# Kernel optimization log

Hardware: AMD Instinct MI355X
Metric: run time of the kernel (lower is better)

Reference implementation:

```python
import jax, jax.numpy as jnp
import numpy as np
import math

B, L, D = 2, 2048, 768
H, DK = 8, 64
DV = D // H  # 96
N_POS = 32
DFF = 2 * D
EPS = 1e-5


def setup_inputs() -> dict:
    key = jax.random.key(0)
    ks = jax.random.split(key, 12)
    s = 0.02
    return {
        "x": jax.random.normal(ks[0], (B, L, D), jnp.float32),
        "norm1_w": jnp.ones((D,), jnp.float32),
        "norm2_w": jnp.ones((D,), jnp.float32),
        "wq": jax.random.normal(ks[1], (D, H * DK), jnp.float32) * s,
        "wk": jax.random.normal(ks[2], (D, H * DK), jnp.float32) * s,
        "wv": jax.random.normal(ks[3], (D, H * DV), jnp.float32) * s,
        "wo": jax.random.normal(ks[4], (H * DV, D), jnp.float32) * s,
        "bo": jnp.zeros((D,), jnp.float32),
        "u_param": jax.random.normal(ks[5], (H, DK), jnp.float32) * s,
        "v_param": jax.random.normal(ks[6], (H, DK), jnp.float32) * s,
        "w_pos": jax.random.normal(ks[7], (H, DK, N_POS), jnp.float32) * s,
        "w1": jax.random.normal(ks[8], (D, DFF), jnp.float32) * s,
        "b1": jnp.zeros((DFF,), jnp.float32),
        "w2": jax.random.normal(ks[9], (DFF, D), jnp.float32) * s,
        "b2": jnp.zeros((D,), jnp.float32),
    }


def _rel_basis(l: int, n: int) -> jnp.ndarray:
    # Enformer-style central-mask relative position basis: [l, l, n]
    pos = jnp.arange(l)
    distance = pos[None, :] - pos[:, None]  # [l, l]
    pow_rate = jnp.exp(jnp.log(jnp.float32((l + 1) / 2.0)) / (n // 2))
    center_widths = pow_rate ** jnp.arange(1, n // 2 + 1, dtype=jnp.float32)
    d = distance[:, :, None].astype(jnp.float32)
    unsigned = (jnp.abs(d) <= center_widths).astype(jnp.float32)
    signed = jnp.sign(d) * unsigned
    return jnp.concatenate([unsigned, signed], axis=-1)  # [l, l, n]


def _rmsnorm(x, w):
    norm = jnp.mean(x * x, axis=-1, keepdims=True)
    return x * jax.lax.rsqrt(norm + EPS) * w


def reference(x, norm1_w, norm2_w, wq, wk, wv, wo, bo,
              u_param, v_param, w_pos, w1, b1, w2, b2):
    b, l, _ = x.shape
    skip = x
    h1 = _rmsnorm(x, norm1_w)

    q = (h1 @ wq).reshape(b, l, H, DK)
    k = (h1 @ wk).reshape(b, l, H, DK)
    v = (h1 @ wv).reshape(b, l, H, DV)

    basis = _rel_basis(l, N_POS)  # [l, l, n]
    scale = 1.0 / math.sqrt(DK)

    # qr_term: contract q with w_pos first, then with basis (avoids [h,l,l,d] r)
    qw = jnp.einsum('bihd,hdn->bihn', q, w_pos)          # [b,l,h,n]
    qr = jnp.einsum('bihn,ijn->bhij', qw, basis)          # [b,h,l,l]
    uk = jnp.einsum('hd,bjhd->bhj', u_param, k)[:, :, None, :]  # [b,h,1,l]
    vw = jnp.einsum('hd,hdn->hn', v_param, w_pos)         # [h,n]
    vr = jnp.einsum('hn,ijn->hij', vw, basis)[None]       # [1,h,l,l]

    bias = (qr + uk + vr) * scale
    scores = jnp.einsum('bihd,bjhd->bhij', q, k) * scale + bias
    attn = jax.nn.softmax(scores, axis=-1)
    out = jnp.einsum('bhij,bjhd->bihd', attn, v)          # [b,l,h,dv]

    out = out.reshape(b, l, H * DV) @ wo + bo
    x = out + skip

    skip = x
    h2 = _rmsnorm(x, norm2_w)
    h2 = jax.nn.gelu(h2 @ w1 + b1, approximate=False) @ w2 + b2
    return h2 + skip
```

## Files before the change

kernel.cpp:

```cpp
#include <hip/hip_runtime.h>

#define B_ 2
#define L_ 2048
#define D_ 768
#define H_ 8
#define DK_ 64
#define DV_ 96
#define NPOS_ 32

typedef __attribute__((ext_vector_type(8))) __bf16 bf16x8;
typedef __attribute__((ext_vector_type(4))) __bf16 bf16x4;
typedef __attribute__((ext_vector_type(4))) float f32x4;

static __device__ __forceinline__ float bs2f(short s) {
    return (float)__builtin_bit_cast(__bf16, s);
}
static __device__ __forceinline__ short f2bs(float f) {
    return __builtin_bit_cast(short, (__bf16)f);
}

__global__ __launch_bounds__(256) void prep_kernel(
    const float* __restrict__ wq, const float* __restrict__ wk,
    const float* __restrict__ wv, const float* __restrict__ wo,
    const float* __restrict__ w1, const float* __restrict__ w2,
    const float* __restrict__ vparam, const float* __restrict__ uparam,
    const float* __restrict__ wpos,
    short* __restrict__ wqkvT, short* __restrict__ woT,
    short* __restrict__ w1T, short* __restrict__ w2T,
    unsigned char* __restrict__ sidx, float* __restrict__ VU, float* __restrict__ VS,
    const float* __restrict__ x, const float* __restrict__ n1w, short* __restrict__ h1)
{
    __shared__ short T[64][66];
    __shared__ float vw[H_ * NPOS_];
    __shared__ float uw[H_ * NPOS_];
    __shared__ float red[4];
    int blk = blockIdx.x, tid = threadIdx.x;
    if (blk < 1056) {
        const float* W; short* Wt; int K, N, bx, by;
        if (blk < 96)       { W = wq; Wt = wqkvT;              K = 768;  N = 512;  int b = blk;       bx = b % 8;  by = b / 8; }
        else if (blk < 192) { W = wk; Wt = wqkvT + 512 * 768;  K = 768;  N = 512;  int b = blk - 96;  bx = b % 8;  by = b / 8; }
        else if (blk < 336) { W = wv; Wt = wqkvT + 1024 * 768; K = 768;  N = 768;  int b = blk - 192; bx = b % 12; by = b / 12; }
        else if (blk < 480) { W = wo; Wt = woT;                K = 768;  N = 768;  int b = blk - 336; bx = b % 12; by = b / 12; }
        else if (blk < 768) { W = w1; Wt = w1T;                K = 768;  N = 1536; int b = blk - 480; bx = b % 24; by = b / 24; }
        else                { W = w2; Wt = w2T;                K = 1536; N = 768;  int b = blk - 768; bx = b % 12; by = b / 12; }
        int n0 = bx << 6, k0 = by << 6;
        for (int idx = tid; idx < 4096; idx += 256) {
            int r = idx >> 6, c = idx & 63;
            T[c][r] = f2bs(W[(size_t)(k0 + r) * N + n0 + c]);
        }
        __syncthreads();
        for (int idx = tid; idx < 4096; idx += 256) {
            int r = idx >> 6, c = idx & 63;
            Wt[(size_t)(n0 + r) * K + k0 + c] = T[r][c];
        }
    } else if (blk == 1056) {
        float pr = expf(logf((L_ + 1) / 2.0f) / (NPOS_ / 2));
        for (int idx = tid; idx < 4095; idx += 256) {
            int d = idx - 2047;
            int ad = d < 0 ? -d : d;
            int c = 0;
            for (int m = 1; m <= NPOS_ / 2; ++m) {
                float cw = powf(pr, (float)m);
                if (cw < (float)ad) c++;
            }
            sidx[idx] = (unsigned char)(d > 0 ? c : (d < 0 ? 17 + c : 34));
        }
        {
            int h = tid >> 5, n = tid & 31;
            float av = 0.f, au = 0.f;
            for (int d = 0; d < DK_; ++d) {
                float wp = wpos[(h * DK_ + d) * NPOS_ + n];
                av += vparam[h * DK_ + d] * wp;
                au += uparam[h * DK_ + d] * wp;
            }
            vw[tid] = av;
            uw[tid] = au;
        }
        __syncthreads();
        if (tid < H_ * 17) {
            int h = tid / 17, m = tid % 17;
            float su = 0.f, ss = 0.f;
            for (int t2 = m; t2 < 16; ++t2) {
                su += vw[h * NPOS_ + t2] - uw[h * NPOS_ + t2];
                ss += vw[h * NPOS_ + 16 + t2] - uw[h * NPOS_ + 16 + t2];
            }
            VU[h * 17 + m] = su * 0.125f;
            VS[h * 17 + m] = ss * 0.125f;
        }
    } else {
        int row = blk - 1057;
        const float* xr = x + (size_t)row * D_;
        float ss = 0.f;
        for (int c = tid; c < D_; c += 256) { float f = xr[c]; ss += f * f; }
        for (int msk = 1; msk < 64; msk <<= 1) ss += __shfl_xor(ss, msk);
        if ((tid & 63) == 0) red[tid >> 6] = ss;
        __syncthreads();
        float tot = red[0] + red[1] + red[2] + red[3];
        float sc = rsqrtf(tot * (1.f / D_) + 1e-5f);
        for (int c = tid; c < D_; c += 256)
            h1[(size_t)row * D_ + c] = f2bs(xr[c] * sc * n1w[c]);
    }
}

__global__ __launch_bounds__(256) void rmsnorm_kernel(
    const float* __restrict__ x, const float* __restrict__ wgt, short* __restrict__ out)
{
    int row = blockIdx.x, tid = threadIdx.x;
    __shared__ float red[4];
    const float* xr = x + (size_t)row * D_;
    float ss = 0.f;
    for (int c = tid; c < D_; c += 256) { float f = xr[c]; ss += f * f; }
    for (int msk = 1; msk < 64; msk <<= 1) ss += __shfl_xor(ss, msk);
    if ((tid & 63) == 0) red[tid >> 6] = ss;
    __syncthreads();
    float tot = red[0] + red[1] + red[2] + red[3];
    float sc = rsqrtf(tot * (1.f / D_) + 1e-5f);
    for (int c = tid; c < D_; c += 256)
        out[(size_t)row * D_ + c] = f2bs(xr[c] * sc * wgt[c]);
}

__global__ __launch_bounds__(256) void gemm64(
    const short* __restrict__ A, const short* __restrict__ Bt,
    const float* __restrict__ bias, const float* __restrict__ resid,
    void* __restrict__ outp,
    int M, int N, int K, int act, int out_f32)
{
    __shared__ __align__(16) short Al[64 * 136];
    __shared__ __align__(16) short Bl[64 * 136];
    int tid = threadIdx.x;
    int w = tid >> 6, lane = tid & 63, quad = lane >> 4, t = lane & 15;
    int m0b = blockIdx.y << 6, n0b = blockIdx.x << 6;
    int wr = (w >> 1) << 5, wc = (w & 1) << 5;
    int rA = tid >> 4, c8 = (tid & 15) << 3;
    f32x4 acc[2][2] = {};
    bf16x8 pA[4], pB[4];
#pragma unroll
    for (int it = 0; it < 4; ++it) {
        pA[it] = *(const bf16x8*)&A[(size_t)(m0b + rA + (it << 4)) * K + c8];
        pB[it] = *(const bf16x8*)&Bt[(size_t)(n0b + rA + (it << 4)) * K + c8];
    }
    for (int kb = 0; kb < K; kb += 128) {
        __syncthreads();
#pragma unroll
        for (int it = 0; it < 4; ++it) {
            *(bf16x8*)&Al[(rA + (it << 4)) * 136 + c8] = pA[it];
            *(bf16x8*)&Bl[(rA + (it << 4)) * 136 + c8] = pB[it];
        }
        if (kb + 128 < K) {
#pragma unroll
            for (int it = 0; it < 4; ++it) {
                pA[it] = *(const bf16x8*)&A[(size_t)(m0b + rA + (it << 4)) * K + kb + 128 + c8];
                pB[it] = *(const bf16x8*)&Bt[(size_t)(n0b + rA + (it << 4)) * K + kb + 128 + c8];
            }
        }
        __syncthreads();
#pragma unroll
        for (int ks = 0; ks < 4; ++ks) {
            bf16x8 af0 = *(bf16x8*)&Al[(wr + t) * 136 + (ks << 5) + (quad << 3)];
            bf16x8 af1 = *(bf16x8*)&Al[(wr + 16 + t) * 136 + (ks << 5) + (quad << 3)];
            bf16x8 bf0 = *(bf16x8*)&Bl[(wc + t) * 136 + (ks << 5) + (quad << 3)];
            bf16x8 bf1 = *(bf16x8*)&Bl[(wc + 16 + t) * 136 + (ks << 5) + (quad << 3)];
            acc[0][0] = __builtin_amdgcn_mfma_f32_16x16x32_bf16(af0, bf0, acc[0][0], 0, 0, 0);
            acc[0][1] = __builtin_amdgcn_mfma_f32_16x16x32_bf16(af0, bf1, acc[0][1], 0, 0, 0);
            acc[1][0] = __builtin_amdgcn_mfma_f32_16x16x32_bf16(af1, bf0, acc[1][0], 0, 0, 0);
            acc[1][1] = __builtin_amdgcn_mfma_f32_16x16x32_bf16(af1, bf1, acc[1][1], 0, 0, 0);
        }
    }
#pragma unroll
    for (int ms = 0; ms < 2; ++ms)
#pragma unroll
        for (int ns = 0; ns < 2; ++ns)
#pragma unroll
            for (int r = 0; r < 4; ++r) {
                int row = m0b + wr + (ms << 4) + (quad << 2) + r;
                int col = n0b + wc + (ns << 4) + t;
                float v2 = acc[ms][ns][r];
                if (bias) v2 += bias[col];
                if (act == 1) v2 = 0.5f * v2 * (1.f + erff(v2 * 0.70710678118654752f));
                if (resid) v2 += resid[(size_t)row * N + col];
                if (out_f32) ((float*)outp)[(size_t)row * N + col] = v2;
                else ((short*)outp)[(size_t)row * N + col] = f2bs(v2);
            }
}

__global__ __launch_bounds__(256) void gemm128(
    const short* __restrict__ A, const short* __restrict__ Bt,
    const float* __restrict__ bias, const float* __restrict__ uadd,
    void* __restrict__ outp, int M, int N, int K, int act)
{
    __shared__ __align__(16) short Al[128 * 72];
    __shared__ __align__(16) short Bl[128 * 72];
    int tid = threadIdx.x;
    int w = tid >> 6, lane = tid & 63, quad = lane >> 4, t = lane & 15;
    int m0b = blockIdx.y << 7, n0b = blockIdx.x << 7;
    int wm = (w >> 1) << 6, wn = (w & 1) << 6;
    int r0 = tid >> 3, c8 = (tid & 7) << 3;
    f32x4 acc[4][4] = {};
    bf16x8 pA[4], pB[4];
#pragma unroll
    for (int it = 0; it < 4; ++it) {
        pA[it] = *(const bf16x8*)&A[(size_t)(m0b + r0 + (it << 5)) * K + c8];
        pB[it] = *(const bf16x8*)&Bt[(size_t)(n0b + r0 + (it << 5)) * K + c8];
    }
    for (int kb = 0; kb < K; kb += 64) {
        __syncthreads();
#pragma unroll
        for (int it = 0; it < 4; ++it) {
            *(bf16x8*)&Al[(r0 + (it << 5)) * 72 + c8] = pA[it];
            *(bf16x8*)&Bl[(r0 + (it << 5)) * 72 + c8] = pB[it];
        }
        if (kb + 64 < K) {
#pragma unroll
            for (int it = 0; it < 4; ++it) {
                pA[it] = *(const bf16x8*)&A[(size_t)(m0b + r0 + (it << 5)) * K + kb + 64 + c8];
                pB[it] = *(const bf16x8*)&Bt[(size_t)(n0b + r0 + (it << 5)) * K + kb + 64 + c8];
            }
        }
        __syncthreads();
#pragma unroll
        for (int ks = 0; ks < 2; ++ks) {
            bf16x8 af[4], bf[4];
#pragma unroll
            for (int ms = 0; ms < 4; ++ms)
                af[ms] = *(bf16x8*)&Al[(wm + ms * 16 + t) * 72 + (ks << 5) + (quad << 3)];
#pragma unroll
            for (int ns = 0; ns < 4; ++ns)
                bf[ns] = *(bf16x8*)&Bl[(wn + ns * 16 + t) * 72 + (ks << 5) + (quad << 3)];
#pragma unroll
            for (int ms = 0; ms < 4; ++ms)
#pragma unroll
                for (int ns = 0; ns < 4; ++ns)
                    acc[ms][ns] = __builtin_amdgcn_mfma_f32_16x16x32_bf16(af[ms], bf[ns], acc[ms][ns], 0, 0, 0);
        }
    }
#pragma unroll
    for (int ms = 0; ms < 4; ++ms)
#pragma unroll
        for (int ns = 0; ns < 4; ++ns)
#pragma unroll
            for (int r = 0; r < 4; ++r) {
                int row = m0b + wm + ms * 16 + (quad << 2) + r;
                int col = n0b + wn + ns * 16 + t;
                float v2 = acc[ms][ns][r];
                if (uadd && col < 512) v2 = 0.125f * (v2 + uadd[col]);
                if (bias) v2 += bias[col];
                if (act == 1) v2 = 0.5f * v2 * (1.f + erff(v2 * 0.70710678118654752f));
                ((short*)outp)[(size_t)row * N + col] = f2bs(v2);
            }
}

__global__ __launch_bounds__(256) void qv_kernel(
    const short* __restrict__ qkv, const float* __restrict__ wpos,
    const float* __restrict__ VU, const float* __restrict__ VS,
    float* __restrict__ Tg, short* __restrict__ vT)
{
    __shared__ __align__(16) char arena[69696];
    int blk = blockIdx.x, tid = threadIdx.x;
    if (blk < 256) {
        float* wl   = (float*)arena;
        float* qrow = (float*)(arena + 65536);
        float* qw   = (float*)(arena + 67584);
        float* sU   = (float*)(arena + 68608);
        float* sS   = (float*)(arena + 69152);
        for (int idx = tid; idx < 4096; idx += 256)
            ((float4*)wl)[idx] = ((const float4*)wpos)[idx];
        int r0 = blk << 4;
        int h = tid >> 5, n = tid & 31;
        for (int rr = 0; rr < 16; ++rr) {
            int row = r0 + rr;
            __syncthreads();
            const short* base = qkv + (size_t)row * 1792;
            qrow[tid]       = bs2f(base[tid]);
            qrow[tid + 256] = bs2f(base[tid + 256]);
            __syncthreads();
            float acc = 0.f;
            for (int d = 0; d < DK_; ++d)
                acc += qrow[h * DK_ + d] * wl[(h * DK_ + d) * 32 + n];
            qw[tid] = acc;
            __syncthreads();
            if (tid < 136) {
                int hh = tid / 17, m = tid % 17;
                float su = 0.f, ss = 0.f;
                for (int t2 = m; t2 < 16; ++t2) { su += qw[hh * NPOS_ + t2]; ss += qw[hh * NPOS_ + 16 + t2]; }
                sU[tid] = su + VU[tid];
                sS[tid] = ss + VS[tid];
            }
            __syncthreads();
            if (tid < 280) {
                int h2 = tid / 35, s = tid % 35;
                int m = s < 17 ? s : (s < 34 ? s - 17 : 0);
                float su = sU[h2 * 17 + m], ss = sS[h2 * 17 + m];
                Tg[(size_t)row * 280 + tid] = s < 17 ? su + ss : (s < 34 ? su - ss : su);
            }
        }
    } else {
        short* T = (short*)arena;
        int vb = blk - 256;
        int bh = vb >> 4, b = bh >> 3, h = bh & 7;
        int j0 = (vb & 15) << 7;
#pragma unroll
        for (int it = 0; it < 6; ++it) {
            int idx = tid + (it << 8);
            int row = idx / 12, c8 = (idx % 12) << 3;
            *(bf16x8*)&T[row * 104 + c8] =
                *(const bf16x8*)&qkv[(size_t)(b * L_ + j0 + row) * 1792 + 1024 + h * DV_ + c8];
        }
        __syncthreads();
#pragma unroll
        for (int it = 0; it < 6; ++it) {
            int idx = tid + (it << 8);
            int sub = idx / 768;
            int rem = idx - sub * 768;
            int f = rem >> 6, l = rem & 63;
            int dv = f >> 1, ks = f & 1;
            int q = l >> 4, t = l & 15;
            bf16x8 o;
#pragma unroll
            for (int e = 0; e < 8; ++e) {
                int jl = ((e & 3) << 4) + (ks << 3) + (q << 1) + (e >> 2);
                o[e] = __builtin_bit_cast(__bf16, T[(sub * 64 + jl) * 104 + dv * 16 + t]);
            }
            int jt = ((vb & 15) << 1) + sub;
            *(bf16x8*)&vT[((((size_t)bh * 32 + jt) * 12 + f) * 64 + l) * 8] = o;
        }
    }
}

__global__ __launch_bounds__(512, 4) void flash_kernel(
    const short* __restrict__ qkv, const short* __restrict__ vT,
    const float* __restrict__ Tg, const unsigned char* __restrict__ sidx_g,
    short* __restrict__ ao)
{
    __shared__ __align__(16) char arena[50176];
    int tid = threadIdx.x;
    int w = tid >> 6, lane = tid & 63, quad = lane >> 4, t = lane & 15;
    int g = w >> 2, wg = w & 3, tg = tid & 255;
    short* Kl = (short*)(arena + g * 18432);
    short* Pl = (short*)(arena + g * 18432 + 9216);
    float* Tt = (float*)(arena + 36864);
    unsigned char* sidxl = (unsigned char*)(arena + 46080);
    int bh = blockIdx.y, b = bh >> 3, h = bh & 7;
    int i0 = blockIdx.x << 6;

    for (int idx = tid; idx < 64 * 35; idx += 512) {
        int il = idx / 35, s = idx % 35;
        Tt[il * 36 + s] = Tg[(size_t)(b * L_ + i0 + il) * 280 + h * 35 + s];
    }
    for (int idx = tid; idx < 4095; idx += 512) sidxl[idx] = sidx_g[idx];

    int iq = i0 + wg * 16 + t;
    const short* qbase = qkv + (size_t)(b * L_ + iq) * 1792 + h * DK_;
    bf16x8 qf0 = *(const bf16x8*)(qbase + (quad << 3));
    bf16x8 qf1 = *(const bf16x8*)(qbase + 32 + (quad << 3));

    f32x4 O[6] = {};
    float lsum[4] = {0.f, 0.f, 0.f, 0.f};

    int kr = tg >> 3, kc = (tg & 7) << 3;
    bf16x8 kpre[2];
    {
        int j0 = g << 6;
        const short* kb0 = &qkv[(size_t)(b * L_ + j0 + kr) * 1792 + 512 + h * DK_ + kc];
        kpre[0] = *(const bf16x8*)kb0;
        kpre[1] = *(const bf16x8*)(kb0 + (size_t)32 * 1792);
    }
    const short* vfb = vT + (size_t)bh * 32 * 12 * 512 + lane * 8;

    for (int tix = 0; tix < 16; ++tix) {
        int j0 = ((tix << 1) + g) << 6;
        int jt = j0 >> 6;
        __syncthreads();
        *(bf16x8*)&Kl[kr * 72 + kc] = kpre[0];
        *(bf16x8*)&Kl[(kr + 32) * 72 + kc] = kpre[1];
        bf16x8 vfrag[12];
#pragma unroll
        for (int f = 0; f < 12; ++f)
            vfrag[f] = *(const bf16x8*)(vfb + ((size_t)jt * 12 + f) * 512);
        {
            int jn = (tix < 15) ? ((((tix + 1) << 1) + g) << 6) : (g << 6);
            const short* kb0 = &qkv[(size_t)(b * L_ + jn + kr) * 1792 + 512 + h * DK_ + kc];
            kpre[0] = *(const bf16x8*)kb0;
            kpre[1] = *(const bf16x8*)(kb0 + (size_t)32 * 1792);
        }
        __syncthreads();

        f32x4 S[4];
        __builtin_amdgcn_s_setprio(1);
#pragma unroll
        for (int ct = 0; ct < 4; ++ct) {
            bf16x8 b0 = *(bf16x8*)&Kl[(ct * 16 + t) * 72 + (quad << 3)];
            bf16x8 b1 = *(bf16x8*)&Kl[(ct * 16 + t) * 72 + 32 + (quad << 3)];
            f32x4 z = {};
            z = __builtin_amdgcn_mfma_f32_16x16x32_bf16(qf0, b0, z, 0, 0, 0);
            S[ct] = __builtin_amdgcn_mfma_f32_16x16x32_bf16(qf1, b1, z, 0, 0, 0);
        }
        __builtin_amdgcn_s_setprio(0);
#pragma unroll
        for (int r = 0; r < 4; ++r) {
            int il = wg * 16 + (quad << 2) + r;
            int i = i0 + il;
            const float* Trow = &Tt[il * 36];
            bf16x4 pv;
#pragma unroll
            for (int ct = 0; ct < 4; ++ct) {
                int j = j0 + ct * 16 + t;
                int s = sidxl[j - i + 2047];
                float p = __expf(S[ct][r] + Trow[s]);
                __bf16 pb = (__bf16)p;
                pv[ct] = pb;
                lsum[r] += (float)pb;
            }
            *(bf16x4*)&Pl[il * 72 + t * 4] = pv;
        }
        __builtin_amdgcn_s_setprio(1);
#pragma unroll
        for (int ks = 0; ks < 2; ++ks) {
            bf16x8 pa = *(bf16x8*)&Pl[(wg * 16 + t) * 72 + (ks << 5) + (quad << 3)];
#pragma unroll
            for (int dv = 0; dv < 6; ++dv)
                O[dv] = __builtin_amdgcn_mfma_f32_16x16x32_bf16(pa, vfrag[dv * 2 + ks], O[dv], 0, 0, 0);
        }
        __builtin_amdgcn_s_setprio(0);
    }

    __syncthreads();
    float* F = (float*)arena;
    int l2 = (wg << 6) + lane;
    if (g == 1) {
#pragma unroll
        for (int dv = 0; dv < 6; ++dv)
#pragma unroll
            for (int r = 0; r < 4; ++r)
                F[((dv << 2) + r) * 256 + l2] = O[dv][r];
#pragma unroll
        for (int r = 0; r < 4; ++r) F[(24 + r) * 256 + l2] = lsum[r];
    }
    __syncthreads();
    if (g == 0) {
#pragma unroll
        for (int r = 0; r < 4; ++r) {
            float lr = lsum[r] + F[(24 + r) * 256 + l2];
            lr += __shfl_xor(lr, 1);
            lr += __shfl_xor(lr, 2);
            lr += __shfl_xor(lr, 4);
            lr += __shfl_xor(lr, 8);
            float inv = 1.f / lr;
            int i = i0 + wg * 16 + (quad << 2) + r;
            size_t base = (size_t)(b * L_ + i) * D_ + h * DV_;
#pragma unroll
            for (int dv = 0; dv < 6; ++dv)
                ao[base + dv * 16 + t] = f2bs((O[dv][r] + F[((dv << 2) + r) * 256 + l2]) * inv);
        }
    }
}

extern "C" void kernel_launch(void* const* d_in, const int* in_sizes, int n_in,
                              void* d_out, int out_size, void* d_ws, size_t ws_size,
                              hipStream_t stream)
{
    const float* x    = (const float*)d_in[0];
    const float* n1w  = (const float*)d_in[1];
    const float* n2w  = (const float*)d_in[2];
    const float* wq   = (const float*)d_in[3];
    const float* wk   = (const float*)d_in[4];
    const float* wv   = (const float*)d_in[5];
    const float* wo   = (const float*)d_in[6];
    const float* bo   = (const float*)d_in[7];
    const float* up   = (const float*)d_in[8];
    const float* vp   = (const float*)d_in[9];
    const float* wpos = (const float*)d_in[10];
    const float* w1   = (const float*)d_in[11];
    const float* b1   = (const float*)d_in[12];
    const float* w2   = (const float*)d_in[13];
    const float* b2   = (const float*)d_in[14];

    char* ws = (char*)d_ws;
    short* h1   = (short*)(ws + 0);
    short* qkv  = (short*)(ws + 6291456);
    float* Tg   = (float*)(ws + 20971520);
    float* VUg  = (float*)(ws + 25559040);
    float* VSg  = (float*)(ws + 25560064);
    unsigned char* sidx = (unsigned char*)(ws + 25561088);
    short* ao   = (short*)(ws + 25569280);
    float* x2   = (float*)(ws + 31860736);
    short* vT   = (short*)(ws + 31860736);
    short* wqkvT= (short*)(ws + 44443648);
    short* woT  = (short*)(ws + 47196160);
    short* w1T  = (short*)(ws + 48375808);
    short* w2T  = (short*)(ws + 50735104);
    short* f1   = (short*)(ws + 0);
    short* h2n  = (short*)(ws + 14680064);

    prep_kernel<<<5153, 256, 0, stream>>>(wq, wk, wv, wo, w1, w2, vp, up, wpos,
                                          wqkvT, woT, w1T, w2T, sidx, VUg, VSg,
                                          x, n1w, h1);
    gemm128<<<dim3(14, 32), 256, 0, stream>>>(h1, wqkvT, nullptr, up, qkv, 4096, 1792, 768, 0);
    qv_kernel<<<512, 256, 0, stream>>>(qkv, wpos, VUg, VSg, Tg, vT);
    flash_kernel<<<dim3(32, 16), 512, 0, stream>>>(qkv, vT, Tg, sidx, ao);
    gemm64<<<dim3(12, 64), 256, 0, stream>>>(ao, woT, bo, x, x2, 4096, 768, 768, 0, 1);
    rmsnorm_kernel<<<4096, 256, 0, stream>>>(x2, n2w, h2n);
    gemm128<<<dim3(12, 32), 256, 0, stream>>>(h2n, w1T, b1, nullptr, f1, 4096, 1536, 768, 1);
    gemm64<<<dim3(12, 64), 256, 0, stream>>>(f1, w2T, b2, x2, d_out, 4096, 768, 1536, 0, 1);
}
```

Baseline: 309.1 us.

## Pre-swizzle K into MFMA fragment layout and drop LDS staging in flash kernel

Adds a K-transpose pass to qv_kernel that writes K in MFMA B-fragment order, so flash_kernel loads K fragments straight from global memory instead of staging them through LDS. This removes the per-tile __syncthreads and LDS writes for K. The flash kernel also shrinks to 256 threads with 32 query rows per block and a swizzled 1D grid that interleaves heads. The costs are an extra global write/read pass for K, more redundant global K loads across blocks, and twice as many blocks.

```diff
diff --git a/kernel.cpp b/kernel.cpp
--- a/kernel.cpp
+++ b/kernel.cpp
@@ -252,7 +252,7 @@
 __global__ __launch_bounds__(256) void qv_kernel(
     const short* __restrict__ qkv, const float* __restrict__ wpos,
     const float* __restrict__ VU, const float* __restrict__ VS,
-    float* __restrict__ Tg, short* __restrict__ vT)
+    float* __restrict__ Tg, short* __restrict__ vT, short* __restrict__ kT)
 {
     __shared__ __align__(16) char arena[69696];
     int blk = blockIdx.x, tid = threadIdx.x;
@@ -293,7 +293,7 @@
                 Tg[(size_t)row * 280 + tid] = s < 17 ? su + ss : (s < 34 ? su - ss : su);
             }
         }
-    } else {
+    } else if (blk < 512) {
         short* T = (short*)arena;
         int vb = blk - 256;
         int bh = vb >> 4, b = bh >> 3, h = bh & 7;
@@ -323,83 +323,101 @@
             int jt = ((vb & 15) << 1) + sub;
             *(bf16x8*)&vT[((((size_t)bh * 32 + jt) * 12 + f) * 64 + l) * 8] = o;
         }
-    }
-}
-
-__global__ __launch_bounds__(512, 4) void flash_kernel(
-    const short* __restrict__ qkv, const short* __restrict__ vT,
-    const float* __restrict__ Tg, const unsigned char* __restrict__ sidx_g,
-    short* __restrict__ ao)
-{
-    __shared__ __align__(16) char arena[50176];
+    } else {
+        short* T = (short*)arena;
+        int vb = blk - 512;
+        int bh = vb >> 4, b = bh >> 3, h = bh & 7;
+        int c128 = vb & 15;
+        int j0 = c128 << 7;
+#pragma unroll
+        for (int it = 0; it < 4; ++it) {
+            int idx = tid + (it << 8);
+            int row = idx >> 3, c8 = (idx & 7) << 3;
+            *(bf16x8*)&T[row * 72 + c8] =
+                *(const bf16x8*)&qkv[(size_t)(b * L_ + j0 + row) * 1792 + 512 + h * DK_ + c8];
+        }
+        __syncthreads();
+#pragma unroll
+        for (int it = 0; it < 4; ++it) {
+            int idx = tid + (it << 8);
+            int sub = idx >> 9;
+            int rem = idx & 511;
+            int f = rem >> 6, l = rem & 63;
+            int q = l >> 4, tt = l & 15;
+            bf16x8 o = *(bf16x8*)&T[(sub * 64 + (f >> 1) * 16 + tt) * 72 + ((f & 1) << 5) + (q << 3)];
+            int jt = (c128 << 1) + sub;
+            *(bf16x8*)&kT[((((size_t)bh * 32 + jt) * 8 + f) * 64 + l) * 8] = o;
+        }
+    }
+}
+
+__global__ __launch_bounds__(256, 4) void flash_kernel(
+    const short* __restrict__ qkv, const short* __restrict__ kT,
+    const short* __restrict__ vT, const float* __restrict__ Tg,
+    const unsigned char* __restrict__ sidx_g, short* __restrict__ ao)
+{
+    __shared__ __align__(16) char arena[17920];
     int tid = threadIdx.x;
     int w = tid >> 6, lane = tid & 63, quad = lane >> 4, t = lane & 15;
-    int g = w >> 2, wg = w & 3, tg = tid & 255;
-    short* Kl = (short*)(arena + g * 18432);
-    short* Pl = (short*)(arena + g * 18432 + 9216);
-    float* Tt = (float*)(arena + 36864);
-    unsigned char* sidxl = (unsigned char*)(arena + 46080);
-    int bh = blockIdx.y, b = bh >> 3, h = bh & 7;
-    int i0 = blockIdx.x << 6;
-
-    for (int idx = tid; idx < 64 * 35; idx += 512) {
-        int il = idx / 35, s = idx % 35;
+    int iw = w >> 1, jg = w & 1;
+    short* Pl = (short*)(arena + w * 2304);
+    float* Tt = (float*)(arena + 9216);
+    unsigned char* sidxl = (unsigned char*)(arena + 13824);
+
+    int id = blockIdx.x;
+    int bh8 = id & 7, rest = id >> 3;
+    int x = rest & 63, hi = rest >> 6;
+    int bh = bh8 + (hi << 3);
+    int b = bh >> 3, h = bh & 7;
+    int i0 = x << 5;
+
+    for (int idx = tid; idx < 32 * 35; idx += 256) {
+        int il = idx / 35, s = idx - il * 35;
         Tt[il * 36 + s] = Tg[(size_t)(b * L_ + i0 + il) * 280 + h * 35 + s];
     }
-    for (int idx = tid; idx < 4095; idx += 512) sidxl[idx] = sidx_g[idx];
-
-    int iq = i0 + wg * 16 + t;
+    for (int idx = tid; idx < 4095; idx += 256) sidxl[idx] = sidx_g[idx];
+    __syncthreads();
+
+    int iq = i0 + iw * 16 + t;
     const short* qbase = qkv + (size_t)(b * L_ + iq) * 1792 + h * DK_;
     bf16x8 qf0 = *(const bf16x8*)(qbase + (quad << 3));
     bf16x8 qf1 = *(const bf16x8*)(qbase + 32 + (quad << 3));
 
     f32x4 O[6] = {};
     float lsum[4] = {0.f, 0.f, 0.f, 0.f};
-
-    int kr = tg >> 3, kc = (tg & 7) << 3;
-    bf16x8 kpre[2];
-    {
-        int j0 = g << 6;
-        const short* kb0 = &qkv[(size_t)(b * L_ + j0 + kr) * 1792 + 512 + h * DK_ + kc];
-        kpre[0] = *(const bf16x8*)kb0;
-        kpre[1] = *(const bf16x8*)(kb0 + (size_t)32 * 1792);
-    }
+    const short* kfb = kT + (size_t)bh * 32 * 8 * 512 + lane * 8;
     const short* vfb = vT + (size_t)bh * 32 * 12 * 512 + lane * 8;
 
     for (int tix = 0; tix < 16; ++tix) {
-        int j0 = ((tix << 1) + g) << 6;
-        int jt = j0 >> 6;
-        __syncthreads();
-        *(bf16x8*)&Kl[kr * 72 + kc] = kpre[0];
-        *(bf16x8*)&Kl[(kr + 32) * 72 + kc] = kpre[1];
-        bf16x8 vfrag[12];
-#pragma unroll
-        for (int f = 0; f < 12; ++f)
-            vfrag[f] = *(const bf16x8*)(vfb + ((size_t)jt * 12 + f) * 512);
-        {
-            int jn = (tix < 15) ? ((((tix + 1) << 1) + g) << 6) : (g << 6);
-            const short* kb0 = &qkv[(size_t)(b * L_ + jn + kr) * 1792 + 512 + h * DK_ + kc];
-            kpre[0] = *(const bf16x8*)kb0;
-            kpre[1] = *(const bf16x8*)(kb0 + (size_t)32 * 1792);
-        }
-        __syncthreads();
+        int jt = (tix << 1) + jg;
+        int j0 = jt << 6;
+        bf16x8 kf[8];
+#pragma unroll
+        for (int f = 0; f < 8; ++f)
+            kf[f] = *(const bf16x8*)(kfb + ((size_t)jt * 8 + f) * 512);
+        __builtin_amdgcn_sched_barrier(0);
 
         f32x4 S[4];
         __builtin_amdgcn_s_setprio(1);
 #pragma unroll
         for (int ct = 0; ct < 4; ++ct) {
-            bf16x8 b0 = *(bf16x8*)&Kl[(ct * 16 + t) * 72 + (quad << 3)];
-            bf16x8 b1 = *(bf16x8*)&Kl[(ct * 16 + t) * 72 + 32 + (quad << 3)];
             f32x4 z = {};
-            z = __builtin_amdgcn_mfma_f32_16x16x32_bf16(qf0, b0, z, 0, 0, 0);
-            S[ct] = __builtin_amdgcn_mfma_f32_16x16x32_bf16(qf1, b1, z, 0, 0, 0);
+            z = __builtin_amdgcn_mfma_f32_16x16x32_bf16(qf0, kf[ct * 2], z, 0, 0, 0);
+            S[ct] = __builtin_amdgcn_mfma_f32_16x16x32_bf16(qf1, kf[ct * 2 + 1], z, 0, 0, 0);
         }
         __builtin_amdgcn_s_setprio(0);
+
+        bf16x8 vf[12];
+#pragma unroll
+        for (int f = 0; f < 12; ++f)
+            vf[f] = *(const bf16x8*)(vfb + ((size_t)jt * 12 + f) * 512);
+        __builtin_amdgcn_sched_barrier(0);
+
 #pragma unroll
         for (int r = 0; r < 4; ++r) {
-            int il = wg * 16 + (quad << 2) + r;
-            int i = i0 + il;
-            const float* Trow = &Tt[il * 36];
+            int il = (quad << 2) + r;
+            int i = i0 + iw * 16 + il;
+            const float* Trow = &Tt[(iw * 16 + il) * 36];
             bf16x4 pv;
 #pragma unroll
             for (int ct = 0; ct < 4; ++ct) {
@@ -415,41 +433,41 @@
         __builtin_amdgcn_s_setprio(1);
 #pragma unroll
         for (int ks = 0; ks < 2; ++ks) {
-            bf16x8 pa = *(bf16x8*)&Pl[(wg * 16 + t) * 72 + (ks << 5) + (quad << 3)];
+            bf16x8 pa = *(bf16x8*)&Pl[t * 72 + (ks << 5) + (quad << 3)];
 #pragma unroll
             for (int dv = 0; dv < 6; ++dv)
-                O[dv] = __builtin_amdgcn_mfma_f32_16x16x32_bf16(pa, vfrag[dv * 2 + ks], O[dv], 0, 0, 0);
+                O[dv] = __builtin_amdgcn_mfma_f32_16x16x32_bf16(pa, vf[dv * 2 + ks], O[dv], 0, 0, 0);
         }
         __builtin_amdgcn_s_setprio(0);
     }
 
     __syncthreads();
     float* F = (float*)arena;
-    int l2 = (wg << 6) + lane;
-    if (g == 1) {
+    int fl = (iw << 6) + lane;
+    if (jg == 1) {
 #pragma unroll
         for (int dv = 0; dv < 6; ++dv)
 #pragma unroll
             for (int r = 0; r < 4; ++r)
-                F[((dv << 2) + r) * 256 + l2] = O[dv][r];
-#pragma unroll
-        for (int r = 0; r < 4; ++r) F[(24 + r) * 256 + l2] = lsum[r];
+                F[((dv << 2) + r) * 128 + fl] = O[dv][r];
+#pragma unroll
+        for (int r = 0; r < 4; ++r) F[(24 + r) * 128 + fl] = lsum[r];
     }
     __syncthreads();
-    if (g == 0) {
+    if (jg == 0) {
 #pragma unroll
         for (int r = 0; r < 4; ++r) {
-            float lr = lsum[r] + F[(24 + r) * 256 + l2];
+            float lr = lsum[r] + F[(24 + r) * 128 + fl];
             lr += __shfl_xor(lr, 1);
             lr += __shfl_xor(lr, 2);
             lr += __shfl_xor(lr, 4);
             lr += __shfl_xor(lr, 8);
             float inv = 1.f / lr;
-            int i = i0 + wg * 16 + (quad << 2) + r;
+            int i = i0 + iw * 16 + (quad << 2) + r;
             size_t base = (size_t)(b * L_ + i) * D_ + h * DV_;
 #pragma unroll
             for (int dv = 0; dv < 6; ++dv)
-                ao[base + dv * 16 + t] = f2bs((O[dv][r] + F[((dv << 2) + r) * 256 + l2]) * inv);
+                ao[base + dv * 16 + t] = f2bs((O[dv][r] + F[((dv << 2) + r) * 128 + fl]) * inv);
         }
     }
 }
@@ -484,6 +502,7 @@
     short* ao   = (short*)(ws + 25569280);
     float* x2   = (float*)(ws + 31860736);
     short* vT   = (short*)(ws + 31860736);
+    short* kT   = (short*)(ws + 38152192);
     short* wqkvT= (short*)(ws + 44443648);
     short* woT  = (short*)(ws + 47196160);
     short* w1T  = (short*)(ws + 48375808);
@@ -495,8 +514,8 @@
                                           wqkvT, woT, w1T, w2T, sidx, VUg, VSg,
                                           x, n1w, h1);
     gemm128<<<dim3(14, 32), 256, 0, stream>>>(h1, wqkvT, nullptr, up, qkv, 4096, 1792, 768, 0);
-    qv_kernel<<<512, 256, 0, stream>>>(qkv, wpos, VUg, VSg, Tg, vT);
-    flash_kernel<<<dim3(32, 16), 512, 0, stream>>>(qkv, vT, Tg, sidx, ao);
+    qv_kernel<<<768, 256, 0, stream>>>(qkv, wpos, VUg, VSg, Tg, vT, kT);
+    flash_kernel<<<dim3(1024), 256, 0, stream>>>(qkv, kT, vT, Tg, sidx, ao);
     gemm64<<<dim3(12, 64), 256, 0, stream>>>(ao, woT, bo, x, x2, 4096, 768, 768, 0, 1);
     rmsnorm_kernel<<<4096, 256, 0, stream>>>(x2, n2w, h2n);
     gemm128<<<dim3(12, 32), 256, 0, stream>>>(h2n, w1T, b1, nullptr, f1, 4096, 1536, 768, 1);
```

Measured after the change: 307.9 us. Within noise of the previous version (-0.4%).
